# Kernel optimization log

Measured on AMD Instinct MI355X. Metric: run time of the kernel, lower is better.

The kernel has to match this reference:

```python
import jax, jax.numpy as jnp
import numpy as np

N = 50000          # residues
E = 1000000        # edges
H = 128            # hidden_channels
CUT = 11.5         # cutoff
NR = 6             # num_radial
NS = 3             # num_spherical
NPE = 16           # num_pos_emb

def swish(x):
    return x * jax.nn.sigmoid(x)

def rbf(d):
    # Bessel-style radial basis with smooth cosine cutoff, [E, NR]
    u = jnp.clip(d / CUT, 0.0, 1.0)
    n = jnp.arange(1, NR + 1, dtype=jnp.float32)
    fc = 0.5 * (jnp.cos(jnp.pi * u) + 1.0)
    return jnp.sqrt(2.0 / CUT) * jnp.sin(n * jnp.pi * u[:, None]) / (d[:, None] + 1e-6) * fc[:, None]

def angle_emb(d, ang):
    # d_angle_emb: radial x cos(l*angle) -> [E, NR*NS]
    r = rbf(d)
    l = jnp.arange(NS, dtype=jnp.float32)
    a = jnp.cos(ang[:, None] * l)
    return (r[:, :, None] * a[:, None, :]).reshape(d.shape[0], NR * NS)

def theta_phi_emb(d, theta, phi):
    # d_theta_phi_emb: radial x angular(theta) x angular(phi) -> [E, NR*NS*NS]
    r = rbf(d)
    l = jnp.arange(NS, dtype=jnp.float32)
    ct = jnp.cos(theta[:, None] * l)
    cp = jnp.cos(phi[:, None] * l)
    return jnp.einsum('en,el,em->enlm', r, ct, cp).reshape(d.shape[0], NR * NS * NS)


def setup_inputs():
    key = jax.random.key(0)
    ks = jax.random.split(key, 20)
    f32 = jnp.float32
    pos = jax.random.normal(ks[0], (N, 3), f32) * 8.0
    pos_n = pos + jax.random.normal(ks[1], (N, 3), f32) * 0.8
    pos_c = pos + jax.random.normal(ks[2], (N, 3), f32) * 0.8
    z = jax.random.randint(ks[3], (N,), 0, 26)
    bb_embs = jax.random.normal(ks[4], (N, 6), f32)
    side_chain_embs = jax.random.normal(ks[5], (N, 8), f32)
    esm_embs = jax.random.normal(ks[6], (N, 1280), f32)
    batch = jnp.zeros((N,), jnp.int32)
    edge_index = jax.random.randint(ks[7], (2, E), 0, N)
    def w(k, shape):
        return jax.random.normal(k, shape, f32) * (1.0 / np.sqrt(shape[0]))
    edge_in = NR * NS * NS + 3 * NR * NS + NPE  # 54 + 54 + 16 = 124
    params = dict(
        W_emb=w(ks[8], (26 + 6 + 8, H // 2)), b_emb=jnp.zeros((H // 2,), f32),
        W_esm=w(ks[9], (1280, H // 2)), b_esm=jnp.zeros((H // 2,), f32),
        W_edge=w(ks[10], (edge_in, H)),
        W_msg=w(ks[11], (H, H)),
        W_upd=w(ks[12], (H, H)),
        W_o0=w(ks[13], (H, H)), b_o0=jnp.zeros((H,), f32),
        W_o1=w(ks[14], (H, 32)), b_o1=jnp.zeros((32,), f32),
        W_of=w(ks[15], (32, 1)), b_of=jnp.zeros((1,), f32),
        W_n0=w(ks[16], (H, 32)), b_n0=jnp.zeros((32,), f32),
        W_nf=w(ks[17], (32, 2)), b_nf=jnp.zeros((2,), f32),
    )
    return dict(z=z, pos=pos, pos_n=pos_n, pos_c=pos_c, bb_embs=bb_embs,
                side_chain_embs=side_chain_embs, esm_embs=esm_embs,
                batch=batch, edge_index=edge_index, **params)


def reference(z, pos, pos_n, pos_c, bb_embs, side_chain_embs, esm_embs, batch,
              edge_index, W_emb, b_emb, W_esm, b_esm, W_edge, W_msg, W_upd,
              W_o0, b_o0, W_o1, b_o1, W_of, b_of, W_n0, b_n0, W_nf, b_nf):
    # --- node embedding fusion (level='allatom+esm') ---
    oh = jax.nn.one_hot(z, 26, dtype=jnp.float32)
    x_a = jnp.concatenate([oh, bb_embs, side_chain_embs], axis=1) @ W_emb + b_emb
    x_s = esm_embs @ W_esm + b_esm
    x = jnp.concatenate([x_a, x_s], axis=-1)  # [N, H]

    j, i = edge_index[0], edge_index[1]

    # --- sinusoidal positional embedding of sequence offsets ---
    dpe = (j - i).astype(jnp.float32)
    freq = jnp.exp(jnp.arange(0, NPE, 2, dtype=jnp.float32) * (-np.log(10000.0) / NPE))
    ang = dpe[:, None] * freq
    pe = jnp.concatenate([jnp.cos(ang), jnp.sin(ang)], axis=-1)  # [E, NPE]

    # --- distance / theta / phi (triplet gathers via sequence neighbors) ---
    v_ji = pos[j] - pos[i]
    dist = jnp.linalg.norm(pos[i] - pos[j], axis=1)
    refi0 = (i - 1) % N
    refi1 = (i + 1) % N
    v_r0 = pos[refi0] - pos[i]
    v_r1 = pos[refi1] - pos[i]
    a = jnp.sum(v_ji * v_r0, axis=-1)
    b = jnp.linalg.norm(jnp.cross(v_ji, v_r0), axis=-1)
    theta = jnp.arctan2(b, a)
    p1 = jnp.cross(v_r0, v_r1)
    p2 = jnp.cross(v_r0, v_ji)
    a = jnp.sum(p1 * p2, axis=-1)
    b = jnp.sum(jnp.cross(p1, p2) * v_r0, axis=-1) / (jnp.linalg.norm(v_r0, axis=-1) + 1e-7)
    phi = jnp.arctan2(b, a)
    feature0 = theta_phi_emb(dist, theta, phi)  # [E, 54]

    # --- backbone-frame Euler angles (allatom branch) ---
    o1x = pos_n[i] - pos[i]
    o1z = jnp.cross(o1x, jnp.cross(o1x, pos_c[i] - pos[i]))
    o1zl = jnp.linalg.norm(o1z, axis=1) + 1e-7
    o2x = pos_n[j] - pos[j]
    o2z = jnp.cross(o2x, jnp.cross(o2x, pos_c[j] - pos[j]))
    o2zl = jnp.linalg.norm(o2z, axis=1) + 1e-7
    nvec = jnp.cross(o1z, o2z)
    angle1 = jnp.arctan2(jnp.sum(jnp.cross(o1x, nvec) * o1z, -1) / o1zl, jnp.sum(o1x * nvec, -1))
    angle2 = jnp.arctan2(jnp.linalg.norm(nvec, axis=-1), jnp.sum(o1z * o2z, -1))
    angle3 = jnp.arctan2(jnp.sum(jnp.cross(nvec, o2x) * o2z, -1) / o2zl, jnp.sum(nvec * o2x, -1))
    feature1 = jnp.concatenate([angle_emb(dist, angle1), angle_emb(dist, angle2),
                                angle_emb(dist, angle3)], axis=1)  # [E, 54]

    # --- message passing (gather-compute-scatter stand-in for model_E) ---
    ef = swish(jnp.concatenate([feature0, feature1, pe], axis=-1) @ W_edge)  # [E, H]
    m = swish(x[j] @ W_msg) * ef
    agg = jax.ops.segment_sum(m, i, num_segments=N)
    xe = x + swish(agg @ W_upd)

    # --- output heads (dropout inactive at inference) ---
    xn = jax.nn.relu(x @ W_n0 + b_n0)
    node_out = xn @ W_nf + b_nf                   # [N, 2]
    h = jax.nn.relu(xe @ W_o0 + b_o0)
    h = jax.nn.relu(h @ W_o1 + b_o1)
    out = jax.nn.sigmoid(h @ W_of + b_of)         # [N, 1]
    return out, node_out
```

## Files before the change

### kernel.cpp

```cpp
#include <hip/hip_runtime.h>
#include <math.h>
#include <stdint.h>

#define NRES 50000
#define NEDGE 1000000
#define PI_F 3.14159265358979323846f
#define NSEG 196

typedef __attribute__((ext_vector_type(8))) short short8;
typedef __attribute__((ext_vector_type(4))) float floatx4;
typedef __attribute__((ext_vector_type(2))) short bf16x2;
typedef __attribute__((address_space(1))) bf16x2* gbf16x2p;

struct f3 { float x, y, z; };
__device__ __forceinline__ f3 ld3(const float* __restrict__ p, int i) {
  return {p[3*i+0], p[3*i+1], p[3*i+2]};
}
__device__ __forceinline__ f3 f3sub(f3 a, f3 b){ return {a.x-b.x, a.y-b.y, a.z-b.z}; }
__device__ __forceinline__ f3 f3cross(f3 a, f3 b){
  return {a.y*b.z - a.z*b.y, a.z*b.x - a.x*b.z, a.x*b.y - a.y*b.x};
}
__device__ __forceinline__ float f3dot(f3 a, f3 b){ return a.x*b.x + a.y*b.y + a.z*b.z; }
__device__ __forceinline__ float swish_fast(float v){
  return v * __builtin_amdgcn_rcpf(1.0f + __expf(-v));
// ... 23 lines not shown
  float ct, cp, ca1, ca2, ca3;
  float dpe;
};
__device__ __forceinline__ EdgeGeo edge_geo(
    int j, int i,
    const float* __restrict__ pos, const float* __restrict__ posn,
    const float* __restrict__ posc)
{
  EdgeGeo g;
  f3 pj = ld3(pos, j), pi = ld3(pos, i);
  f3 vji = f3sub(pj, pi);
  float nji2 = f3dot(vji, vji);
  float dist = sqrtf(nji2);
  int r0i = (i == 0) ? (NRES - 1) : (i - 1);
  int r1i = (i == NRES - 1) ? 0 : (i + 1);
  f3 vr0 = f3sub(ld3(pos, r0i), pi);
  f3 vr1 = f3sub(ld3(pos, r1i), pi);
  float nr02 = f3dot(vr0, vr0);

  g.ct = f3dot(vji, vr0) * __builtin_amdgcn_rsqf(fmaxf(nji2 * nr02, 1e-30f));
  f3 p1 = f3cross(vr0, vr1);
  f3 p2 = f3cross(vr0, vji);
  float pa = f3dot(p1, p2);
  float pb = f3dot(f3cross(p1, p2), vr0) / (sqrtf(nr02) + 1e-7f);
  g.cp = cos_atan2(pb, pa);

  f3 pni = ld3(posn, i), pci = ld3(posc, i);
  f3 o1x = f3sub(pni, pi);
  f3 o1z = f3cross(o1x, f3cross(o1x, f3sub(pci, pi)));
  float no1z2 = f3dot(o1z, o1z);
  float o1zl = sqrtf(no1z2) + 1e-7f;
  f3 pnj = ld3(posn, j), pcj = ld3(posc, j);
  f3 o2x = f3sub(pnj, pj);
  f3 o2z = f3cross(o2x, f3cross(o2x, f3sub(pcj, pj)));
  float no2z2 = f3dot(o2z, o2z);
  float o2zl = sqrtf(no2z2) + 1e-7f;
  f3 nv = f3cross(o1z, o2z);
  float y1 = f3dot(f3cross(o1x, nv), o1z) / o1zl;
  g.ca1 = cos_atan2(y1, f3dot(o1x, nv));
  g.ca2 = f3dot(o1z, o2z) * __builtin_amdgcn_rsqf(fmaxf(no1z2 * no2z2, 1e-30f));
  float y3 = f3dot(f3cross(nv, o2x), o2z) / o2zl;
  g.ca3 = cos_atan2(y3, f3dot(nv, o2x));

  float u = fminf(dist * (1.0f/11.5f), 1.0f);
  float spu, cpu;
  __sincosf(PI_F * u, &spu, &cpu);
  float fc = 0.5f * (cpu + 1.0f);
  float pref = 0.41702882811414954f * __builtin_amdgcn_rcpf(dist + 1e-6f) * fc;
  {
    float twoc = 2.0f * cpu;
    float s_nm1 = 0.0f, s_n = spu;
    #pragma unroll
    for (int nn = 0; nn < 6; ++nn) {
      g.rb[nn] = pref * s_n;
      float s_np1 = twoc * s_n - s_nm1;
      s_nm1 = s_n; s_n = s_np1;
    }
  }
  g.dpe = (float)(j - i);
  return g;
}

__device__ __forceinline__ float feat_val(const EdgeGeo& g, int f,
                                          const float* ctv, const float* cpv,
                                          const float* cav1, const float* cav2,
                                          const float* cav3)
{
  if (f < 54) {
    int nn = f / 9, l = (f % 9) / 3, m = f % 3;
    return g.rb[nn] * ctv[l] * cpv[m];
  } else {
    int ff = f - 54;
    int t = ff / 18, nn = (ff % 18) / 3, l = ff % 3;
    const float* cav = (t == 0) ? cav1 : (t == 1) ? cav2 : cav3;
    return g.rb[nn] * cav[l];
  }
}

__device__ __forceinline__ void expand_q(
    const EdgeGeo& g, int e, int q, short (*sF)[136])
{
  float ctv[3]  = {1.0f, g.ct,  2.0f*g.ct*g.ct  - 1.0f};
  float cpv[3]  = {1.0f, g.cp,  2.0f*g.cp*g.cp  - 1.0f};
  float cav1[3] = {1.0f, g.ca1, 2.0f*g.ca1*g.ca1 - 1.0f};
  float cav2[3] = {1.0f, g.ca2, 2.0f*g.ca2*g.ca2 - 1.0f};
  float cav3[3] = {1.0f, g.ca3, 2.0f*g.ca3*g.ca3 - 1.0f};

  if (q == 0) {
    #pragma unroll
    for (int f = 0; f < 28; f += 2)
      *(unsigned*)&sF[e][f] = pkbf(feat_val(g, f, ctv, cpv, cav1, cav2, cav3),
                                   feat_val(g, f+1, ctv, cpv, cav1, cav2, cav3));
  } else if (q == 1) {
    #pragma unroll
    for (int f = 28; f < 54; f += 2)
      *(unsigned*)&sF[e][f] = pkbf(feat_val(g, f, ctv, cpv, cav1, cav2, cav3),
                                   feat_val(g, f+1, ctv, cpv, cav1, cav2, cav3));
    const float FRQ[8] = {1.0f, 0.31622776601683794f, 0.1f, 0.03162277660168379f,
                          0.01f, 0.003162277660168379f, 0.001f, 0.0003162277660168379f};
    float cb[8], sb[8];
    #pragma unroll
    for (int p = 0; p < 8; ++p) __sincosf(g.dpe * FRQ[p], &sb[p], &cb[p]);
    #pragma unroll
    for (int p = 0; p < 8; p += 2) {
      *(unsigned*)&sF[e][108 + p] = pkbf(cb[p], cb[p+1]);
      *(unsigned*)&sF[e][116 + p] = pkbf(sb[p], sb[p+1]);
    }
    *(unsigned*)&sF[e][124] = 0u;
    *(unsigned*)&sF[e][126] = 0u;
  } else if (q == 2) {
    #pragma unroll
    for (int f = 54; f < 80; f += 2)
      *(unsigned*)&sF[e][f] = pkbf(feat_val(g, f, ctv, cpv, cav1, cav2, cav3),
                                   feat_val(g, f+1, ctv, cpv, cav1, cav2, cav3));
  } else {
    #pragma unroll
    for (int f = 80; f < 108; f += 2)
      *(unsigned*)&sF[e][f] = pkbf(feat_val(g, f, ctv, cpv, cav1, cav2, cav3),
                                   feat_val(g, f+1, ctv, cpv, cav1, cav2, cav3));
  }
}

__device__ __forceinline__ void edge_features_full(
    int e, int j, int i,
    const float* __restrict__ pos, const float* __restrict__ posn,
    const float* __restrict__ posc, short (*sF)[136])
{
  EdgeGeo g = edge_geo(j, i, pos, posn, posc);
  float ctv[3]  = {1.0f, g.ct,  2.0f*g.ct*g.ct  - 1.0f};
  float cpv[3]  = {1.0f, g.cp,  2.0f*g.cp*g.cp  - 1.0f};
  float cav1[3] = {1.0f, g.ca1, 2.0f*g.ca1*g.ca1 - 1.0f};
  float cav2[3] = {1.0f, g.ca2, 2.0f*g.ca2*g.ca2 - 1.0f};
  float cav3[3] = {1.0f, g.ca3, 2.0f*g.ca3*g.ca3 - 1.0f};
  #pragma unroll
  for (int f = 0; f < 108; f += 2) {
    float v0 = feat_val(g, f,     ctv, cpv, cav1, cav2, cav3);
    float v1 = feat_val(g, f + 1, ctv, cpv, cav1, cav2, cav3);
    *(unsigned*)&sF[e][f] = pkbf(v0, v1);
  }
  const float FRQ[8] = {1.0f, 0.31622776601683794f, 0.1f, 0.03162277660168379f,
                        0.01f, 0.003162277660168379f, 0.001f, 0.0003162277660168379f};
  float cb[8], sb[8];
  #pragma unroll
  for (int q = 0; q < 8; ++q) __sincosf(g.dpe * FRQ[q], &sb[q], &cb[q]);
  #pragma unroll
  for (int q = 0; q < 8; q += 2) {
    *(unsigned*)&sF[e][108 + q] = pkbf(cb[q], cb[q+1]);
    *(unsigned*)&sF[e][116 + q] = pkbf(sb[q], sb[q+1]);
  }
  *(unsigned*)&sF[e][124] = 0u;
  *(unsigned*)&sF[e][126] = 0u;
}

__global__ __launch_bounds__(256) void k_wprep(
    const float* __restrict__ We, const float* __restrict__ Wm,
    const float* __restrict__ Ws, const float* __restrict__ Wu,
    const float* __restrict__ Wo0, const float* __restrict__ Wn0,
    const float* __restrict__ Wo1,
    short* __restrict__ Wef, short* __restrict__ Wmf, short* __restrict__ Wsf,
    short* __restrict__ Wuf, short* __restrict__ Wo0f,
    short* __restrict__ Wn0f, short* __restrict__ Wo1f)
{
  int gid = blockIdx.x * 256 + threadIdx.x;
  const float* src; short* dst; int NT, K, N, t;
  if      (gid < 16384)  { t = gid;          src = We;  dst = Wef;  NT = 8; K = 124;  N = 128; }
  else if (gid < 32768)  { t = gid - 16384;  src = Wm;  dst = Wmf;  NT = 8; K = 128;  N = 128; }
  else if (gid < 114688) { t = gid - 32768;  src = Ws;  dst = Wsf;  NT = 4; K = 1280; N = 64;  }
  else if (gid < 131072) { t = gid - 114688; src = Wu;  dst = Wuf;  NT = 8; K = 128;  N = 128; }
  else if (gid < 147456) { t = gid - 131072; src = Wo0; dst = Wo0f; NT = 8; K = 128;  N = 128; }
  else if (gid < 151552) { t = gid - 147456; src = Wn0; dst = Wn0f; NT = 2; K = 128;  N = 32;  }
  else if (gid < 155648) { t = gid - 151552; src = Wo1; dst = Wo1f; NT = 2; K = 128;  N = 32;  }
  else return;
  int j = t & 7, lane = (t >> 3) & 63;
  int rest = t >> 9;
  int nt = rest % NT, kt = rest / NT;
  int k = kt*32 + (lane >> 4)*8 + j, n = nt*16 + (lane & 15);
  dst[t] = f2bf((k < K) ? src[k*N + n] : 0.0f);
}

__global__ __launch_bounds__(256) void k_hist(
    const int* __restrict__ ei, int* __restrict__ bins)
{
  int e = blockIdx.x * 256 + threadIdx.x;
  if (e < NEDGE) atomicAdd(&bins[ei[NEDGE + e]], 1);
}

__global__ __launch_bounds__(256) void k_scan1(
    int* __restrict__ bins, int* __restrict__ bsum)
{
  __shared__ int s[256];
  const int t = threadIdx.x, b = blockIdx.x;
  const int idx = b * 256 + t;
  int v = (idx < NRES) ? bins[idx] : 0;
  s[t] = v;
  __syncthreads();
  #pragma unroll
  for (int d = 1; d < 256; d <<= 1) {
    int add = (t >= d) ? s[t - d] : 0;
    __syncthreads();
    if (t >= d) s[t] += add;
    __syncthreads();
  }
  if (idx < NRES) bins[idx] = s[t] - v;
  if (t == 255) bsum[b] = s[255];
}

__global__ __launch_bounds__(256) void k_scan2(int* __restrict__ bsum)
{
  __shared__ int s[256];
  const int t = threadIdx.x;
  int v = (t < NSEG) ? bsum[t] : 0;
  s[t] = v;
  __syncthreads();
  #pragma unroll
  for (int d = 1; d < 256; d <<= 1) {
    int add = (t >= d) ? s[t - d] : 0;
    __syncthreads();
    if (t >= d) s[t] += add;
    __syncthreads();
  }
  if (t < NSEG) bsum[t] = s[t] - v;
}

__global__ __launch_bounds__(256) void k_scatter(
    const int* __restrict__ ei, int* __restrict__ bins,
    const int* __restrict__ bsum, int2* __restrict__ sij)
{
  int e = blockIdx.x * 256 + threadIdx.x;
  if (e < NEDGE) {
    int j = ei[e], i = ei[NEDGE + e];
    int slot = atomicAdd(&bins[i], 1) + bsum[i >> 8];
    if (slot >= 0 && slot < NEDGE) sij[slot] = make_int2(j, i);
  }
}

__global__ __launch_bounds__(256) void k_xa(
    const int* __restrict__ z, const float* __restrict__ bb,
    const float* __restrict__ side, const float* __restrict__ W_emb,
    const float* __restrict__ b_emb, short* __restrict__ xb)
{
  int tid = threadIdx.x;
  int h = tid & 63;
  int n = blockIdx.x * 4 + (tid >> 6);
  if (n >= NRES) return;
  int zz = z[n];
  float acc = W_emb[zz * 64 + h] + b_emb[h];
  #pragma unroll
  for (int k = 0; k < 6; ++k) acc += bb[n*6 + k] * W_emb[(26 + k)*64 + h];
  #pragma unroll
  for (int k = 0; k < 8; ++k) acc += side[n*8 + k] * W_emb[(32 + k)*64 + h];
  xb[(size_t)n * 128 + h] = f2bf(acc);
}

__global__ __launch_bounds__(256) void k_esm(
    const float* __restrict__ esm, const short* __restrict__ Wsf,
    const float* __restrict__ b, short* __restrict__ xb)
{
  const int tid = threadIdx.x;
  const int lane = tid & 63, w = tid >> 6;
  const int quad = lane >> 4, colb = lane & 15;
  const int tile0 = blockIdx.x * 64 + w * 16;

  int arow = tile0 + colb;
  if (arow >= NRES) arow = NRES - 1;
  const float* ap = esm + (size_t)arow * 1280 + quad * 8;

  floatx4 acc[4];
  #pragma unroll
  for (int nt = 0; nt < 4; ++nt) acc[nt] = (floatx4){0.f, 0.f, 0.f, 0.f};

  for (int kt = 0; kt < 40; ++kt) {
    float4 v0 = *(const float4*)(ap + kt*32);
    float4 v1 = *(const float4*)(ap + kt*32 + 4);
    short8 a;
    a[0] = f2bf(v0.x); a[1] = f2bf(v0.y); a[2] = f2bf(v0.z); a[3] = f2bf(v0.w);
    a[4] = f2bf(v1.x); a[5] = f2bf(v1.y); a[6] = f2bf(v1.z); a[7] = f2bf(v1.w);
    #pragma unroll
    for (int nt = 0; nt < 4; ++nt) {
      short8 bf = *(const short8*)&Wsf[(size_t)((kt*4 + nt)*64 + lane)*8];
      acc[nt] = __builtin_amdgcn_mfma_f32_16x16x32_bf16(a, bf, acc[nt], 0, 0, 0);
    }
  }
  #pragma unroll
  for (int nt = 0; nt < 4; ++nt) {
    int ch = nt*16 + colb;
    float bias = b[ch];
    #pragma unroll
    for (int r = 0; r < 4; ++r) {
      int n = tile0 + quad*4 + r;
      if (n < NRES) xb[(size_t)n * 128 + 64 + ch] = f2bf(acc[nt][r] + bias);
    }
  }
}

__global__ __launch_bounds__(512) void k_node(
    const float* __restrict__ esm, const short* __restrict__ Wsf,
    const float* __restrict__ b_esm,
    const int* __restrict__ z, const float* __restrict__ bb,
    const float* __restrict__ side, const float* __restrict__ W_emb,
    const float* __restrict__ b_emb,
    const short* __restrict__ Wmf,
    short* __restrict__ xb, short* __restrict__ xmb)
{
  __shared__ __align__(16) short sE[2][64][72];
  __shared__ __align__(16) short sX[64][136];

  const int tid = threadIdx.x;
  const int lane = tid & 63, w = tid >> 6;
  const int quad = lane >> 4, colb = lane & 15;
  const int n0 = blockIdx.x * 64;

  const int lrow = tid >> 3;
  const int p0 = tid & 7, p1 = p0 + 8;
  int grow = n0 + lrow; if (grow >= NRES) grow = NRES - 1;
  const float* rbase = esm + (size_t)grow * 1280;

  const int rt = w & 3;
  const int ct0 = (w >> 2) * 2, ct1 = ct0 + 1;

  floatx4 acc0 = (floatx4){0.f,0.f,0.f,0.f};
  floatx4 acc1 = (floatx4){0.f,0.f,0.f,0.f};

  {
    float4 va = *(const float4*)(rbase + p0*4);
    float4 vb = *(const float4*)(rbase + p1*4);
    *(unsigned*)&sE[0][lrow][p0*4]     = pkbf(va.x, va.y);
    *(unsigned*)&sE[0][lrow][p0*4 + 2] = pkbf(va.z, va.w);
    *(unsigned*)&sE[0][lrow][p1*4]     = pkbf(vb.x, vb.y);
    *(unsigned*)&sE[0][lrow][p1*4 + 2] = pkbf(vb.z, vb.w);
  }
  __syncthreads();

  for (int s = 0; s < 20; ++s) {
    float4 va = {0.f,0.f,0.f,0.f}, vb = {0.f,0.f,0.f,0.f};
    if (s < 19) {
      va = *(const float4*)(rbase + (s+1)*64 + p0*4);
      vb = *(const float4*)(rbase + (s+1)*64 + p1*4);
    }
    const int buf = s & 1;
    #pragma unroll
    for (int kk = 0; kk < 2; ++kk) {
      short8 af = *(const short8*)&sE[buf][rt*16 + colb][kk*32 + quad*8];
      const int kc = s*2 + kk;
      short8 bf0 = *(const short8*)&Wsf[(size_t)((kc*4 + ct0)*64 + lane)*8];
      short8 bf1 = *(const short8*)&Wsf[(size_t)((kc*4 + ct1)*64 + lane)*8];
      acc0 = __builtin_amdgcn_mfma_f32_16x16x32_bf16(af, bf0, acc0, 0, 0, 0);
      acc1 = __builtin_amdgcn_mfma_f32_16x16x32_bf16(af, bf1, acc1, 0, 0, 0);
    }
    if (s < 19) {
      const int nb = (s + 1) & 1;
      *(unsigned*)&sE[nb][lrow][p0*4]     = pkbf(va.x, va.y);
      *(unsigned*)&sE[nb][lrow][p0*4 + 2] = pkbf(va.z, va.w);
      *(unsigned*)&sE[nb][lrow][p1*4]     = pkbf(vb.x, vb.y);
      *(unsigned*)&sE[nb][lrow][p1*4 + 2] = pkbf(vb.z, vb.w);
    }
    __syncthreads();
  }

  {
    float bias0 = b_esm[ct0*16 + colb];
    float bias1 = b_esm[ct1*16 + colb];
    #pragma unroll
    for (int r = 0; r < 4; ++r) {
      int row = rt*16 + quad*4 + r;
      sX[row][64 + ct0*16 + colb] = f2bf(acc0[r] + bias0);
      sX[row][64 + ct1*16 + colb] = f2bf(acc1[r] + bias1);
    }
  }
  {
    int r2 = tid >> 3;
    int n2 = n0 + r2; if (n2 >= NRES) n2 = NRES - 1;
    int c0 = (tid & 7) * 8;
    int zz = z[n2];
    float bbv[6], sdv[8];
    #pragma unroll
    for (int k = 0; k < 6; ++k) bbv[k] = bb[n2*6 + k];
    #pragma unroll
    for (int k = 0; k < 8; ++k) sdv[k] = side[n2*8 + k];
    #pragma unroll
    for (int c = 0; c < 8; c += 2) {
      float u0, u1;
      #pragma unroll
      for (int h = 0; h < 2; ++h) {
        int col = c0 + c + h;
        float a2 = W_emb[zz*64 + col] + b_emb[col];
        #pragma unroll
        for (int k = 0; k < 6; ++k) a2 += bbv[k] * W_emb[(26 + k)*64 + col];
        #pragma unroll
        for (int k = 0; k < 8; ++k) a2 += sdv[k] * W_emb[(32 + k)*64 + col];
        if (h) u1 = a2; else u0 = a2;
      }
      *(unsigned*)&sX[r2][c0 + c] = pkbf(u0, u1);
    }
  }
  __syncthreads();

  #pragma unroll
  for (int it = 0; it < 2; ++it) {
    int idx = it * 512 + tid;
    int row = idx >> 4, c8 = idx & 15;
    int n = n0 + row;
    if (n < NRES) *(short8*)&xb[(size_t)n * 128 + c8*8] = *(const short8*)&sX[row][c8*8];
  }

  floatx4 accM[4];
  #pragma unroll
  for (int mt = 0; mt < 4; ++mt) accM[mt] = (floatx4){0.f,0.f,0.f,0.f};
  #pragma unroll
  for (int kt = 0; kt < 4; ++kt) {
    short8 b0 = *(const short8*)&Wmf[(size_t)((kt*8 + w)*64 + lane)*8];
    #pragma unroll
    for (int mt = 0; mt < 4; ++mt) {
      short8 a = *(const short8*)&sX[mt*16 + colb][kt*32 + quad*8];
      accM[mt] = __builtin_amdgcn_mfma_f32_16x16x32_bf16(a, b0, accM[mt], 0, 0, 0);
    }
  }
  __syncthreads();

  #pragma unroll
  for (int mt = 0; mt < 4; ++mt)
    #pragma unroll
    for (int r = 0; r < 4; ++r)
      sX[mt*16 + quad*4 + r][w*16 + colb] = f2bf(swish_fast(accM[mt][r]));
  __syncthreads();
  #pragma unroll
  for (int it = 0; it < 2; ++it) {
    int idx = it * 512 + tid;
    int row = idx >> 4, c8 = idx & 15;
    int n = n0 + row;
    if (n < NRES) *(short8*)&xmb[(size_t)n * 128 + c8*8] = *(const short8*)&sX[row][c8*8];
  }
}

__global__ __launch_bounds__(256, 4) void k_edge_s(
    const int2* __restrict__ sij,
    const float* __restrict__ pos,
    const float* __restrict__ posn, const float* __restrict__ posc,
    const short* __restrict__ xmb, const short* __restrict__ Wef,
    short* __restrict__ aggb)
{
  __shared__ int sJ[64];
  __shared__ int sI[64];
  __shared__ float sG[64][15];
  __shared__ __align__(16) short sF[64][136];
  __shared__ __align__(16) short sXJ[64][136];

  const int tid = threadIdx.x;
  const int orig = blockIdx.x;
  const int xcd = orig & 7, sub = orig >> 3;
  const int wg = (xcd == 0 ? 0 : 1954 + (xcd - 1) * 1953) + sub;
  const int e0 = wg * 64;

  if (tid < 64) {
    int2 ji = sij[e0 + tid];
    int jj = ji.x, ii = ji.y;
    sJ[tid] = (jj < 0) ? 0 : ((jj >= NRES) ? NRES - 1 : jj);
    sI[tid] = (ii < 0) ? 0 : ((ii >= NRES) ? NRES - 1 : ii);
  }
  __syncthreads();

  if (tid < 64) {
    EdgeGeo g = edge_geo(sJ[tid], sI[tid], pos, posn, posc);
    #pragma unroll
    for (int k = 0; k < 6; ++k) sG[tid][k] = g.rb[k];
    sG[tid][6] = g.ct;  sG[tid][7] = g.cp;
    sG[tid][8] = g.ca1; sG[tid][9] = g.ca2; sG[tid][10] = g.ca3;
    sG[tid][11] = g.dpe;
  } else {
    const int t2 = tid - 64;
    for (int it = 0; it < 6; ++it) {
      int idx = it * 192 + t2;
      if (idx < 1024) {
        int row = idx >> 4;
        int c8 = idx & 15;
        *(short8*)&sXJ[row][c8*8] = *(const short8*)&xmb[(size_t)sJ[row] * 128 + c8*8];
      }
    }
  }
  __syncthreads();

  {
    const int e = tid & 63, q = tid >> 6;
    EdgeGeo g;
    #pragma unroll
    for (int k = 0; k < 6; ++k) g.rb[k] = sG[e][k];
    g.ct  = sG[e][6];  g.cp  = sG[e][7];
    g.ca1 = sG[e][8];  g.ca2 = sG[e][9]; g.ca3 = sG[e][10];
    g.dpe = sG[e][11];
    expand_q(g, e, q, sF);
  }
  __syncthreads();

  const int lane = tid & 63, w = tid >> 6;
  const int quad = lane >> 4, colb = lane & 15;
  const int nb = w * 2;

  short8 bE[4][2];
  #pragma unroll
  for (int kt = 0; kt < 4; ++kt)
    #pragma unroll
    for (int nt = 0; nt < 2; ++nt)
      bE[kt][nt] = *(const short8*)&Wef[(size_t)((kt*8 + nb + nt)*64 + lane)*8];

  floatx4 accE[4][2];
  #pragma unroll
  for (int mt = 0; mt < 4; ++mt) {
    accE[mt][0] = (floatx4){0.f, 0.f, 0.f, 0.f};
    accE[mt][1] = (floatx4){0.f, 0.f, 0.f, 0.f};
  }

  #pragma unroll
  for (int kt = 0; kt < 4; ++kt) {
    #pragma unroll
    for (int mt = 0; mt < 4; ++mt) {
      short8 af = *(const short8*)&sF[mt*16 + colb][kt*32 + quad*8];
      #pragma unroll
      for (int nt = 0; nt < 2; ++nt)
        accE[mt][nt] = __builtin_amdgcn_mfma_f32_16x16x32_bf16(af, bE[kt][nt], accE[mt][nt], 0, 0, 0);
    }
  }
  __syncthreads();

  short (*sM)[136] = sF;
  #pragma unroll
  for (int mt = 0; mt < 4; ++mt)
    #pragma unroll
    for (int nt = 0; nt < 2; ++nt) {
      int ch = w*32 + nt*16 + colb;
      #pragma unroll
      for (int r = 0; r < 4; ++r) {
        int e = mt*16 + quad*4 + r;
        float mv = bf2f(sXJ[e][ch]) * swish_fast(accE[mt][nt][r]);
        sM[e][ch] = f2bf(mv);
      }
    }
  __syncthreads();

  {
    const int p = tid & 63;
    const int g = tid >> 6;
    float ax = 0.f, ay = 0.f;
    int cur = sI[g * 16];
    #pragma unroll
    for (int rr = 0; rr < 16; ++rr) {
      int row = g * 16 + rr;
      int ii = sI[row];
      if (ii != cur) {
        bf16x2 v; v[0] = f2bf(ax); v[1] = f2bf(ay);
        atom_pk_bf16(&aggb[(size_t)cur * 128 + p*2], v);
        ax = 0.f; ay = 0.f; cur = ii;
      }
      bf16x2 mv = *(const bf16x2*)&sM[row][p*2];
      ax += bf2f(mv[0]); ay += bf2f(mv[1]);
    }
    bf16x2 v; v[0] = f2bf(ax); v[1] = f2bf(ay);
    atom_pk_bf16(&aggb[(size_t)cur * 128 + p*2], v);
  }
}

__global__ __launch_bounds__(256, 4) void k_edge_b(
    const int* __restrict__ ei, const float* __restrict__ pos,
    const float* __restrict__ posn, const float* __restrict__ posc,
    const short* __restrict__ xb, const short* __restrict__ Wef,
    const short* __restrict__ Wmf, short* __restrict__ aggb)
{
  __shared__ int sJ[64];
  __shared__ int sI[64];
  __shared__ __align__(16) short sF[64][136];
  __shared__ __align__(16) short sXJ[64][136];

  const int tid = threadIdx.x;
  const int e0 = blockIdx.x * 64;

  if (tid < 64) { sJ[tid] = ei[e0 + tid]; sI[tid] = ei[NEDGE + e0 + tid]; }
  __syncthreads();

  if (tid < 64) {
    edge_features_full(tid, sJ[tid], sI[tid], pos, posn, posc, sF);
  } else {
    const int t2 = tid - 64;
    for (int it = 0; it < 6; ++it) {
      int idx = it * 192 + t2;
      if (idx < 1024) {
        int row = idx >> 4;
        int c8 = idx & 15;
        *(short8*)&sXJ[row][c8*8] = *(const short8*)&xb[(size_t)sJ[row] * 128 + c8*8];
      }
    }
  }
  __syncthreads();

  const int lane = tid & 63, w = tid >> 6;
  const int quad = lane >> 4, colb = lane & 15;
  const int nb = w * 2;

  short8 bE[4][2], bM[4][2];
  #pragma unroll
  for (int kt = 0; kt < 4; ++kt)
    #pragma unroll
    for (int nt = 0; nt < 2; ++nt) {
      bE[kt][nt] = *(const short8*)&Wef[(size_t)((kt*8 + nb + nt)*64 + lane)*8];
      bM[kt][nt] = *(const short8*)&Wmf[(size_t)((kt*8 + nb + nt)*64 + lane)*8];
    }

  floatx4 accE[4][2], accM[4][2];
  #pragma unroll
  for (int mt = 0; mt < 4; ++mt)
    #pragma unroll
    for (int nt = 0; nt < 2; ++nt) {
      accE[mt][nt] = (floatx4){0.f, 0.f, 0.f, 0.f};
      accM[mt][nt] = (floatx4){0.f, 0.f, 0.f, 0.f};
    }

  #pragma unroll
  for (int kt = 0; kt < 4; ++kt) {
    #pragma unroll
    for (int mt = 0; mt < 4; ++mt) {
      short8 af = *(const short8*)&sF [mt*16 + colb][kt*32 + quad*8];
      short8 ax = *(const short8*)&sXJ[mt*16 + colb][kt*32 + quad*8];
      #pragma unroll
      for (int nt = 0; nt < 2; ++nt) {
        accE[mt][nt] = __builtin_amdgcn_mfma_f32_16x16x32_bf16(af, bE[kt][nt], accE[mt][nt], 0, 0, 0);
        accM[mt][nt] = __builtin_amdgcn_mfma_f32_16x16x32_bf16(ax, bM[kt][nt], accM[mt][nt], 0, 0, 0);
      }
    }
  }
  __syncthreads();

  short (*sM)[136] = sXJ;
  #pragma unroll
  for (int mt = 0; mt < 4; ++mt)
    #pragma unroll
    for (int nt = 0; nt < 2; ++nt) {
      int ch = w*32 + nt*16 + colb;
      #pragma unroll
      for (int r = 0; r < 4; ++r) {
        int e = mt*16 + quad*4 + r;
        sM[e][ch] = f2bf(swish_fast(accM[mt][nt][r]) * swish_fast(accE[mt][nt][r]));
      }
    }
  __syncthreads();

  #pragma unroll
  for (int it = 0; it < 16; ++it) {
    int flat = it * 256 + tid;
    int row = flat >> 6, p = flat & 63;
    bf16x2 v = *(const bf16x2*)&sM[row][p*2];
    atom_pk_bf16(&aggb[(size_t)sI[row] * 128 + p*2], v);
  }
}

__global__ __launch_bounds__(256) void k_upd(
    const short* __restrict__ xb, const short* __restrict__ aggb,
    const short* __restrict__ Wuf, const short* __restrict__ Wo0f,
    const short* __restrict__ Wn0f, const short* __restrict__ Wo1f,
    const float* __restrict__ bn0, const float* __restrict__ Wnf,
    const float* __restrict__ bnf, const float* __restrict__ bo0,
    const float* __restrict__ bo1, const float* __restrict__ Wof,
    const float* __restrict__ bof, float* __restrict__ out0,
    float* __restrict__ out1)
{
  __shared__ __align__(16) short sA[64][136];
  __shared__ __align__(16) short sX[64][136];
  __shared__ float sS[64][33];

  const int tid = threadIdx.x;
  const int lane = tid & 63, w = tid >> 6;
  const int quad = lane >> 4, colb = lane & 15;
  const int n0 = blockIdx.x * 64;

  #pragma unroll
  for (int it = 0; it < 4; ++it) {
    int idx = it * 256 + tid;
    int row = idx >> 4, c8 = idx & 15;
    int n = n0 + row;
    short8 va = (short8)(short)0, vx = (short8)(short)0;
    if (n < NRES) {
      va = *(const short8*)&aggb[(size_t)n * 128 + c8*8];
      vx = *(const short8*)&xb  [(size_t)n * 128 + c8*8];
    }
    *(short8*)&sA[row][c8*8] = va;
    *(short8*)&sX[row][c8*8] = vx;
  }
  __syncthreads();

  {
    floatx4 accN[2];
    accN[0] = (floatx4){0.f,0.f,0.f,0.f}; accN[1] = (floatx4){0.f,0.f,0.f,0.f};
    #pragma unroll
    for (int kt = 0; kt < 4; ++kt) {
      short8 a = *(const short8*)&sX[w*16 + colb][kt*32 + quad*8];
      #pragma unroll
      for (int nt = 0; nt < 2; ++nt) {
        short8 bf = *(const short8*)&Wn0f[(size_t)((kt*2 + nt)*64 + lane)*8];
        accN[nt] = __builtin_amdgcn_mfma_f32_16x16x32_bf16(a, bf, accN[nt], 0, 0, 0);
      }
    }
    #pragma unroll
    for (int nt = 0; nt < 2; ++nt) {
      int col = nt*16 + colb;
      float bias = bn0[col];
      #pragma unroll
      for (int r = 0; r < 4; ++r)
        sS[w*16 + quad*4 + r][col] = fmaxf(accN[nt][r] + bias, 0.0f);
    }
  }
  __syncthreads();
  if (tid < 128) {
    int row = tid >> 1, oc = tid & 1;
    int n = n0 + row;
    if (n < NRES) {
      float a2 = bnf[oc];
      #pragma unroll
      for (int k = 0; k < 32; ++k) a2 += sS[row][k] * Wnf[k*2 + oc];
      out1[(size_t)n * 2 + oc] = a2;
    }
  }

  floatx4 acc1[4][2];
  #pragma unroll
  for (int mt = 0; mt < 4; ++mt) {
    acc1[mt][0] = (floatx4){0.f,0.f,0.f,0.f};
    acc1[mt][1] = (floatx4){0.f,0.f,0.f,0.f};
  }
  #pragma unroll
  for (int kt = 0; kt < 4; ++kt) {
    short8 b0 = *(const short8*)&Wuf[(size_t)((kt*8 + w*2 + 0)*64 + lane)*8];
    short8 b1 = *(const short8*)&Wuf[(size_t)((kt*8 + w*2 + 1)*64 + lane)*8];
    #pragma unroll
    for (int mt = 0; mt < 4; ++mt) {
      short8 a = *(const short8*)&sA[mt*16 + colb][kt*32 + quad*8];
      acc1[mt][0] = __builtin_amdgcn_mfma_f32_16x16x32_bf16(a, b0, acc1[mt][0], 0, 0, 0);
      acc1[mt][1] = __builtin_amdgcn_mfma_f32_16x16x32_bf16(a, b1, acc1[mt][1], 0, 0, 0);
    }
  }
  __syncthreads();
  #pragma unroll
  for (int mt = 0; mt < 4; ++mt)
    #pragma unroll
    for (int nt = 0; nt < 2; ++nt)
      #pragma unroll
      for (int r = 0; r < 4; ++r) {
        int row = mt*16 + quad*4 + r, col = w*32 + nt*16 + colb;
        float xv = bf2f(sX[row][col]);
        sA[row][col] = f2bf(xv + swish_fast(acc1[mt][nt][r]));
      }
  __syncthreads();

  floatx4 acc2[4][2];
  #pragma unroll
  for (int mt = 0; mt < 4; ++mt) {
    acc2[mt][0] = (floatx4){0.f,0.f,0.f,0.f};
    acc2[mt][1] = (floatx4){0.f,0.f,0.f,0.f};
  }
  #pragma unroll
  for (int kt = 0; kt < 4; ++kt) {
    short8 b0 = *(const short8*)&Wo0f[(size_t)((kt*8 + w*2 + 0)*64 + lane)*8];
    short8 b1 = *(const short8*)&Wo0f[(size_t)((kt*8 + w*2 + 1)*64 + lane)*8];
    #pragma unroll
    for (int mt = 0; mt < 4; ++mt) {
      short8 a = *(const short8*)&sA[mt*16 + colb][kt*32 + quad*8];
      acc2[mt][0] = __builtin_amdgcn_mfma_f32_16x16x32_bf16(a, b0, acc2[mt][0], 0, 0, 0);
      acc2[mt][1] = __builtin_amdgcn_mfma_f32_16x16x32_bf16(a, b1, acc2[mt][1], 0, 0, 0);
    }
  }
  __syncthreads();
  #pragma unroll
  for (int mt = 0; mt < 4; ++mt)
    #pragma unroll
    for (int nt = 0; nt < 2; ++nt) {
      int col = w*32 + nt*16 + colb;
      float bias = bo0[col];
      #pragma unroll
      for (int r = 0; r < 4; ++r) {
        int row = mt*16 + quad*4 + r;
        sX[row][col] = f2bf(fmaxf(acc2[mt][nt][r] + bias, 0.0f));
      }
    }
  __syncthreads();

  {
    floatx4 accH[2];
    accH[0] = (floatx4){0.f,0.f,0.f,0.f}; accH[1] = (floatx4){0.f,0.f,0.f,0.f};
    #pragma unroll
    for (int kt = 0; kt < 4; ++kt) {
      short8 a = *(const short8*)&sX[w*16 + colb][kt*32 + quad*8];
      #pragma unroll
      for (int nt = 0; nt < 2; ++nt) {
        short8 bf = *(const short8*)&Wo1f[(size_t)((kt*2 + nt)*64 + lane)*8];
        accH[nt] = __builtin_amdgcn_mfma_f32_16x16x32_bf16(a, bf, accH[nt], 0, 0, 0);
      }
    }
    __syncthreads();
    #pragma unroll
    for (int nt = 0; nt < 2; ++nt) {
      int col = nt*16 + colb;
      float bias = bo1[col];
      #pragma unroll
      for (int r = 0; r < 4; ++r)
        sS[w*16 + quad*4 + r][col] = fmaxf(accH[nt][r] + bias, 0.0f);
    }
  }
  __syncthreads();

  if (tid < 64) {
    int n = n0 + tid;
    if (n < NRES) {
      float a2 = bof[0];
      #pragma unroll
      for (int k = 0; k < 32; ++k) a2 += sS[tid][k] * Wof[k];
      out0[n] = 1.0f / (1.0f + expf(-a2));
    }
  }
}

extern "C" void kernel_launch(void* const* d_in, const int* in_sizes, int n_in,
                              void* d_out, int out_size, void* d_ws, size_t ws_size,
                              hipStream_t stream) {
  (void)in_sizes; (void)n_in; (void)out_size;
  const int*   z     = (const int*)  d_in[0];
  const float* pos   = (const float*)d_in[1];
  const float* posn  = (const float*)d_in[2];
  const float* posc  = (const float*)d_in[3];
  const float* bb    = (const float*)d_in[4];
  const float* side  = (const float*)d_in[5];
  const float* esm   = (const float*)d_in[6];
  const int*   ei    = (const int*)  d_in[8];
  const float* W_emb = (const float*)d_in[9];
  const float* b_emb = (const float*)d_in[10];
  const float* W_esm = (const float*)d_in[11];
  const float* b_esm = (const float*)d_in[12];
  const float* W_edge= (const float*)d_in[13];
  const float* W_msg = (const float*)d_in[14];
  const float* W_upd = (const float*)d_in[15];
  const float* W_o0  = (const float*)d_in[16];
  const float* b_o0  = (const float*)d_in[17];
  const float* W_o1  = (const float*)d_in[18];
  const float* b_o1  = (const float*)d_in[19];
  const float* W_of  = (const float*)d_in[20];
  const float* b_of  = (const float*)d_in[21];
  const float* W_n0  = (const float*)d_in[22];
  const float* b_n0  = (const float*)d_in[23];
  const float* W_nf  = (const float*)d_in[24];
  const float* b_nf  = (const float*)d_in[25];

  float* out0 = (float*)d_out;
  float* out1 = out0 + NRES;
  char* ws = (char*)d_ws;

  const bool full = (ws_size >= (size_t)46912096);

  if (full) {
    short* xb   = (short*)ws;
    short* aggb = (short*)(ws + 12800000);
    short* xmb  = (short*)(ws + 25600000);
    short* Wef  = (short*)(ws + 38400000);
    short* Wmf  = (short*)(ws + 38432768);
    short* Wsf  = (short*)(ws + 38465536);
    short* Wuf  = (short*)(ws + 38629376);
    short* Wo0f = (short*)(ws + 38662144);
    short* Wn0f = (short*)(ws + 38694912);
    short* Wo1f = (short*)(ws + 38703104);
    int*   bins = (int*)  (ws + 38711296);
    int*   bsum = (int*)  (ws + 38911296);
    int2*  sij  = (int2*) (ws + 38912096);

    hipMemsetAsync(aggb, 0, (size_t)NRES * 128 * sizeof(short), stream);
    hipMemsetAsync(bins, 0, (size_t)NRES * sizeof(int), stream);

    k_wprep  <<<608, 256, 0, stream>>>(W_edge, W_msg, W_esm, W_upd, W_o0, W_n0, W_o1,
                                       Wef, Wmf, Wsf, Wuf, Wo0f, Wn0f, Wo1f);
    k_hist   <<<3907, 256, 0, stream>>>(ei, bins);
    k_scan1  <<<NSEG, 256, 0, stream>>>(bins, bsum);
    k_scan2  <<<1,    256, 0, stream>>>(bsum);
    k_scatter<<<3907, 256, 0, stream>>>(ei, bins, bsum, sij);
    k_node   <<<782,  512, 0, stream>>>(esm, Wsf, b_esm, z, bb, side, W_emb, b_emb,
                                        Wmf, xb, xmb);
    k_edge_s <<<15625, 256, 0, stream>>>(sij, pos, posn, posc, xmb, Wef, aggb);
    k_upd    <<<782,   256, 0, stream>>>(xb, aggb, Wuf, Wo0f, Wn0f, Wo1f,
                                         b_n0, W_nf, b_nf, b_o0, b_o1, W_of, b_of,
                                         out0, out1);
  } else {
    short* xb   = (short*)ws;
    short* aggb = (short*)(ws + 12800000);
    short* Wef  = (short*)(ws + 25600000);
    short* Wmf  = (short*)(ws + 25632768);
    short* Wsf  = (short*)(ws + 25665536);
    short* Wuf  = (short*)(ws + 25829376);
    short* Wo0f = (short*)(ws + 25862144);
    short* Wn0f = (short*)(ws + 25894912);
    short* Wo1f = (short*)(ws + 25903104);

    hipMemsetAsync(aggb, 0, (size_t)NRES * 128 * sizeof(short), stream);

    k_wprep <<<608, 256, 0, stream>>>(W_edge, W_msg, W_esm, W_upd, W_o0, W_n0, W_o1,
                                      Wef, Wmf, Wsf, Wuf, Wo0f, Wn0f, Wo1f);
    k_xa    <<<12500, 256, 0, stream>>>(z, bb, side, W_emb, b_emb, xb);
    k_esm   <<<782,   256, 0, stream>>>(esm, Wsf, b_esm, xb);
    k_edge_b<<<15625, 256, 0, stream>>>(ei, pos, posn, posc, xb, Wef, Wmf, aggb);
    k_upd   <<<782,   256, 0, stream>>>(xb, aggb, Wuf, Wo0f, Wn0f, Wo1f,
                                        b_n0, W_nf, b_nf, b_o0, b_o1, W_of, b_of,
                                        out0, out1);
  }
}
```

Before: 679.2 us.

## Fuse hist into wprep, node head into k_node, and double edge tile size

Merges the edge histogram into the weight-prep launch and moves the node output head (W_n0/W_nf) into k_node, where x is already in shared memory, so k_upd_s only computes the update and output path. The edge kernel now processes 128 edges per 512-thread block, with each wave owning one 16-column slice across eight row tiles, and its XCD-aware block remap is adjusted to the new block count. Padding edges get a sentinel index and are skipped during the atomic scatter. This cuts launches and redundant node reads and gives more edges per block for segment-reduction, but the larger shared-memory footprint and lower occupancy could hurt latency hiding.

```diff
diff --git a/kernel.cpp b/kernel.cpp
--- a/kernel.cpp
+++ b/kernel.cpp
@@ -199,6 +199,37 @@
   *(unsigned*)&sF[e][126] = 0u;
 }
 
+__global__ __launch_bounds__(256) void k_wprep_hist(
+    const float* __restrict__ We, const float* __restrict__ Wm,
+    const float* __restrict__ Ws, const float* __restrict__ Wu,
+    const float* __restrict__ Wo0, const float* __restrict__ Wn0,
+    const float* __restrict__ Wo1,
+    short* __restrict__ Wef, short* __restrict__ Wmf, short* __restrict__ Wsf,
+    short* __restrict__ Wuf, short* __restrict__ Wo0f,
+    short* __restrict__ Wn0f, short* __restrict__ Wo1f,
+    const int* __restrict__ ei, int* __restrict__ bins)
+{
+  if (blockIdx.x >= 608) {
+    int e = (blockIdx.x - 608) * 256 + threadIdx.x;
+    if (e < NEDGE) atomicAdd(&bins[ei[NEDGE + e]], 1);
+    return;
+  }
+  int gid = blockIdx.x * 256 + threadIdx.x;
+  const float* src; short* dst; int NT, K, N, t;
+  if      (gid < 16384)  { t = gid;          src = We;  dst = Wef;  NT = 8; K = 124;  N = 128; }
+  else if (gid < 32768)  { t = gid - 16384;  src = Wm;  dst = Wmf;  NT = 8; K = 128;  N = 128; }
+  else if (gid < 114688) { t = gid - 32768;  src = Ws;  dst = Wsf;  NT = 4; K = 1280; N = 64;  }
+  else if (gid < 131072) { t = gid - 114688; src = Wu;  dst = Wuf;  NT = 8; K = 128;  N = 128; }
+  else if (gid < 147456) { t = gid - 131072; src = Wo0; dst = Wo0f; NT = 8; K = 128;  N = 128; }
+  else if (gid < 151552) { t = gid - 147456; src = Wn0; dst = Wn0f; NT = 2; K = 128;  N = 32;  }
+  else                   { t = gid - 151552; src = Wo1; dst = Wo1f; NT = 2; K = 128;  N = 32;  }
+  int j = t & 7, lane = (t >> 3) & 63;
+  int rest = t >> 9;
+  int nt = rest % NT, kt = rest / NT;
+  int k = kt*32 + (lane >> 4)*8 + j, n = nt*16 + (lane & 15);
+  dst[t] = f2bf((k < K) ? src[k*N + n] : 0.0f);
+}
+
 __global__ __launch_bounds__(256) void k_wprep(
     const float* __restrict__ We, const float* __restrict__ Wm,
     const float* __restrict__ Ws, const float* __restrict__ Wu,
@@ -225,13 +256,6 @@
   dst[t] = f2bf((k < K) ? src[k*N + n] : 0.0f);
 }
 
-__global__ __launch_bounds__(256) void k_hist(
-    const int* __restrict__ ei, int* __restrict__ bins)
-{
-  int e = blockIdx.x * 256 + threadIdx.x;
-  if (e < NEDGE) atomicAdd(&bins[ei[NEDGE + e]], 1);
-}
-
 __global__ __launch_bounds__(256) void k_scan1(
     int* __restrict__ bins, int* __restrict__ bsum)
 {
@@ -347,7 +371,10 @@
     const float* __restrict__ side, const float* __restrict__ W_emb,
     const float* __restrict__ b_emb,
     const short* __restrict__ Wmf,
-    short* __restrict__ xb, short* __restrict__ xmb)
+    const short* __restrict__ Wn0f, const float* __restrict__ bn0,
+    const float* __restrict__ Wnf, const float* __restrict__ bnf,
+    short* __restrict__ xb, short* __restrict__ xmb,
+    float* __restrict__ out1)
 {
   __shared__ __align__(16) short sE[2][64][72];
   __shared__ __align__(16) short sX[64][136];
@@ -462,6 +489,23 @@
       accM[mt] = __builtin_amdgcn_mfma_f32_16x16x32_bf16(a, b0, accM[mt], 0, 0, 0);
     }
   }
+
+  float (*sS)[33] = (float(*)[33])&sE[0][0][0];
+  {
+    const int hmt = w & 3, hnt = w >> 2;
+    floatx4 accN = (floatx4){0.f,0.f,0.f,0.f};
+    #pragma unroll
+    for (int kt = 0; kt < 4; ++kt) {
+      short8 a = *(const short8*)&sX[hmt*16 + colb][kt*32 + quad*8];
+      short8 bf = *(const short8*)&Wn0f[(size_t)((kt*2 + hnt)*64 + lane)*8];
+      accN = __builtin_amdgcn_mfma_f32_16x16x32_bf16(a, bf, accN, 0, 0, 0);
+    }
+    int col = hnt*16 + colb;
+    float bias = bn0[col];
+    #pragma unroll
+    for (int r = 0; r < 4; ++r)
+      sS[hmt*16 + quad*4 + r][col] = fmaxf(accN[r] + bias, 0.0f);
+  }
   __syncthreads();
 
   #pragma unroll
@@ -469,6 +513,16 @@
     #pragma unroll
     for (int r = 0; r < 4; ++r)
       sX[mt*16 + quad*4 + r][w*16 + colb] = f2bf(swish_fast(accM[mt][r]));
+  if (tid < 128) {
+    int row = tid >> 1, oc = tid & 1;
+    int n = n0 + row;
+    if (n < NRES) {
+      float a2 = bnf[oc];
+      #pragma unroll
+      for (int k = 0; k < 32; ++k) a2 += sS[row][k] * Wnf[k*2 + oc];
+      out1[(size_t)n * 2 + oc] = a2;
+    }
+  }
   __syncthreads();
   #pragma unroll
   for (int it = 0; it < 2; ++it) {
@@ -479,45 +533,51 @@
   }
 }
 
-__global__ __launch_bounds__(256, 4) void k_edge_s(
+__global__ __launch_bounds__(512, 2) void k_edge_s(
     const int2* __restrict__ sij,
     const float* __restrict__ pos,
     const float* __restrict__ posn, const float* __restrict__ posc,
     const short* __restrict__ xmb, const short* __restrict__ Wef,
     short* __restrict__ aggb)
 {
-  __shared__ int sJ[64];
-  __shared__ int sI[64];
-  __shared__ float sG[64][15];
-  __shared__ __align__(16) short sF[64][136];
-  __shared__ __align__(16) short sXJ[64][136];
+  __shared__ int sJ[128];
+  __shared__ int sI[128];
+  __shared__ float sG[128][15];
+  __shared__ __align__(16) short sF[128][136];
+  __shared__ __align__(16) short sXJ[128][136];
 
   const int tid = threadIdx.x;
   const int orig = blockIdx.x;
   const int xcd = orig & 7, sub = orig >> 3;
-  const int wg = (xcd == 0 ? 0 : 1954 + (xcd - 1) * 1953) + sub;
-  const int e0 = wg * 64;
-
-  if (tid < 64) {
-    int2 ji = sij[e0 + tid];
-    int jj = ji.x, ii = ji.y;
-    sJ[tid] = (jj < 0) ? 0 : ((jj >= NRES) ? NRES - 1 : jj);
-    sI[tid] = (ii < 0) ? 0 : ((ii >= NRES) ? NRES - 1 : ii);
-  }
-  __syncthreads();
-
-  if (tid < 64) {
-    EdgeGeo g = edge_geo(sJ[tid], sI[tid], pos, posn, posc);
+  const int wg = (xcd < 5 ? xcd * 977 : 5*977 + (xcd - 5) * 976) + sub;
+  const int e0 = wg * 128;
+
+  if (tid < 128) {
+    int ee = e0 + tid;
+    if (ee < NEDGE) {
+      int2 ji = sij[ee];
+      int jj = ji.x, ii = ji.y;
+      sJ[tid] = (jj < 0) ? 0 : ((jj >= NRES) ? NRES - 1 : jj);
+      sI[tid] = (ii < 0) ? 0 : ((ii >= NRES) ? NRES - 1 : ii);
+    } else {
+      sJ[tid] = 0; sI[tid] = -1;
+    }
+  }
+  __syncthreads();
+
+  if (tid < 128) {
+    int ii = sI[tid]; if (ii < 0) ii = 0;
+    EdgeGeo g = edge_geo(sJ[tid], ii, pos, posn, posc);
     #pragma unroll
     for (int k = 0; k < 6; ++k) sG[tid][k] = g.rb[k];
     sG[tid][6] = g.ct;  sG[tid][7] = g.cp;
     sG[tid][8] = g.ca1; sG[tid][9] = g.ca2; sG[tid][10] = g.ca3;
     sG[tid][11] = g.dpe;
   } else {
-    const int t2 = tid - 64;
+    const int t2 = tid - 128;
     for (int it = 0; it < 6; ++it) {
-      int idx = it * 192 + t2;
-      if (idx < 1024) {
+      int idx = it * 384 + t2;
+      if (idx < 2048) {
         int row = idx >> 4;
         int c8 = idx & 15;
         *(short8*)&sXJ[row][c8*8] = *(const short8*)&xmb[(size_t)sJ[row] * 128 + c8*8];
@@ -527,7 +587,7 @@
   __syncthreads();
 
   {
-    const int e = tid & 63, q = tid >> 6;
+    const int e = tid & 127, q = tid >> 7;
     EdgeGeo g;
     #pragma unroll
     for (int k = 0; k < 6; ++k) g.rb[k] = sG[e][k];
@@ -540,47 +600,37 @@
 
   const int lane = tid & 63, w = tid >> 6;
   const int quad = lane >> 4, colb = lane & 15;
-  const int nb = w * 2;
-
-  short8 bE[4][2];
+
+  short8 bE[4];
   #pragma unroll
   for (int kt = 0; kt < 4; ++kt)
-    #pragma unroll
-    for (int nt = 0; nt < 2; ++nt)
-      bE[kt][nt] = *(const short8*)&Wef[(size_t)((kt*8 + nb + nt)*64 + lane)*8];
-
-  floatx4 accE[4][2];
-  #pragma unroll
-  for (int mt = 0; mt < 4; ++mt) {
-    accE[mt][0] = (floatx4){0.f, 0.f, 0.f, 0.f};
-    accE[mt][1] = (floatx4){0.f, 0.f, 0.f, 0.f};
-  }
+    bE[kt] = *(const short8*)&Wef[(size_t)((kt*8 + w)*64 + lane)*8];
+
+  floatx4 accE[8];
+  #pragma unroll
+  for (int mt = 0; mt < 8; ++mt) accE[mt] = (floatx4){0.f, 0.f, 0.f, 0.f};
 
   #pragma unroll
   for (int kt = 0; kt < 4; ++kt) {
     #pragma unroll
-    for (int mt = 0; mt < 4; ++mt) {
+    for (int mt = 0; mt < 8; ++mt) {
       short8 af = *(const short8*)&sF[mt*16 + colb][kt*32 + quad*8];
-      #pragma unroll
-      for (int nt = 0; nt < 2; ++nt)
-        accE[mt][nt] = __builtin_amdgcn_mfma_f32_16x16x32_bf16(af, bE[kt][nt], accE[mt][nt], 0, 0, 0);
+      accE[mt] = __builtin_amdgcn_mfma_f32_16x16x32_bf16(af, bE[kt], accE[mt], 0, 0, 0);
     }
   }
   __syncthreads();
 
   short (*sM)[136] = sF;
   #pragma unroll
-  for (int mt = 0; mt < 4; ++mt)
-    #pragma unroll
-    for (int nt = 0; nt < 2; ++nt) {
-      int ch = w*32 + nt*16 + colb;
-      #pragma unroll
-      for (int r = 0; r < 4; ++r) {
-        int e = mt*16 + quad*4 + r;
-        float mv = bf2f(sXJ[e][ch]) * swish_fast(accE[mt][nt][r]);
-        sM[e][ch] = f2bf(mv);
-      }
-    }
+  for (int mt = 0; mt < 8; ++mt) {
+    int ch = w*16 + colb;
+    #pragma unroll
+    for (int r = 0; r < 4; ++r) {
+      int e = mt*16 + quad*4 + r;
+      float mv = bf2f(sXJ[e][ch]) * swish_fast(accE[mt][r]);
+      sM[e][ch] = f2bf(mv);
+    }
+  }
   __syncthreads();
 
   {
@@ -593,15 +643,19 @@
       int row = g * 16 + rr;
       int ii = sI[row];
       if (ii != cur) {
-        bf16x2 v; v[0] = f2bf(ax); v[1] = f2bf(ay);
-        atom_pk_bf16(&aggb[(size_t)cur * 128 + p*2], v);
+        if (cur >= 0) {
+          bf16x2 v; v[0] = f2bf(ax); v[1] = f2bf(ay);
+          atom_pk_bf16(&aggb[(size_t)cur * 128 + p*2], v);
+        }
         ax = 0.f; ay = 0.f; cur = ii;
       }
       bf16x2 mv = *(const bf16x2*)&sM[row][p*2];
       ax += bf2f(mv[0]); ay += bf2f(mv[1]);
     }
-    bf16x2 v; v[0] = f2bf(ax); v[1] = f2bf(ay);
-    atom_pk_bf16(&aggb[(size_t)cur * 128 + p*2], v);
+    if (cur >= 0) {
+      bf16x2 v; v[0] = f2bf(ax); v[1] = f2bf(ay);
+      atom_pk_bf16(&aggb[(size_t)cur * 128 + p*2], v);
+    }
   }
 }
 
@@ -697,7 +751,135 @@
   }
 }
 
-__global__ __launch_bounds__(256) void k_upd(
+__global__ __launch_bounds__(256) void k_upd_s(
+    const short* __restrict__ xb, const short* __restrict__ aggb,
+    const short* __restrict__ Wuf, const short* __restrict__ Wo0f,
+    const short* __restrict__ Wo1f,
+    const float* __restrict__ bo0, const float* __restrict__ bo1,
+    const float* __restrict__ Wof, const float* __restrict__ bof,
+    float* __restrict__ out0)
+{
+  __shared__ __align__(16) short sA[64][136];
+  __shared__ __align__(16) short sX[64][136];
+  __shared__ float sS[64][33];
+
+  const int tid = threadIdx.x;
+  const int lane = tid & 63, w = tid >> 6;
+  const int quad = lane >> 4, colb = lane & 15;
+  const int n0 = blockIdx.x * 64;
+
+  #pragma unroll
+  for (int it = 0; it < 4; ++it) {
+    int idx = it * 256 + tid;
+    int row = idx >> 4, c8 = idx & 15;
+    int n = n0 + row;
+    short8 va = (short8)(short)0, vx = (short8)(short)0;
+    if (n < NRES) {
+      va = *(const short8*)&aggb[(size_t)n * 128 + c8*8];
+      vx = *(const short8*)&xb  [(size_t)n * 128 + c8*8];
+    }
+    *(short8*)&sA[row][c8*8] = va;
+    *(short8*)&sX[row][c8*8] = vx;
+  }
+  __syncthreads();
+
+  floatx4 acc1[4][2];
+  #pragma unroll
+  for (int mt = 0; mt < 4; ++mt) {
+    acc1[mt][0] = (floatx4){0.f,0.f,0.f,0.f};
+    acc1[mt][1] = (floatx4){0.f,0.f,0.f,0.f};
+  }
+  #pragma unroll
+  for (int kt = 0; kt < 4; ++kt) {
+    short8 b0 = *(const short8*)&Wuf[(size_t)((kt*8 + w*2 + 0)*64 + lane)*8];
+    short8 b1 = *(const short8*)&Wuf[(size_t)((kt*8 + w*2 + 1)*64 + lane)*8];
+    #pragma unroll
+    for (int mt = 0; mt < 4; ++mt) {
+      short8 a = *(const short8*)&sA[mt*16 + colb][kt*32 + quad*8];
+      acc1[mt][0] = __builtin_amdgcn_mfma_f32_16x16x32_bf16(a, b0, acc1[mt][0], 0, 0, 0);
+      acc1[mt][1] = __builtin_amdgcn_mfma_f32_16x16x32_bf16(a, b1, acc1[mt][1], 0, 0, 0);
+    }
+  }
+  __syncthreads();
+  #pragma unroll
+  for (int mt = 0; mt < 4; ++mt)
+    #pragma unroll
+    for (int nt = 0; nt < 2; ++nt)
+      #pragma unroll
+      for (int r = 0; r < 4; ++r) {
+        int row = mt*16 + quad*4 + r, col = w*32 + nt*16 + colb;
+        float xv = bf2f(sX[row][col]);
+        sA[row][col] = f2bf(xv + swish_fast(acc1[mt][nt][r]));
+      }
+  __syncthreads();
+
+  floatx4 acc2[4][2];
+  #pragma unroll
+  for (int mt = 0; mt < 4; ++mt) {
+    acc2[mt][0] = (floatx4){0.f,0.f,0.f,0.f};
+    acc2[mt][1] = (floatx4){0.f,0.f,0.f,0.f};
+  }
+  #pragma unroll
+  for (int kt = 0; kt < 4; ++kt) {
+    short8 b0 = *(const short8*)&Wo0f[(size_t)((kt*8 + w*2 + 0)*64 + lane)*8];
+    short8 b1 = *(const short8*)&Wo0f[(size_t)((kt*8 + w*2 + 1)*64 + lane)*8];
+    #pragma unroll
+    for (int mt = 0; mt < 4; ++mt) {
+      short8 a = *(const short8*)&sA[mt*16 + colb][kt*32 + quad*8];
+      acc2[mt][0] = __builtin_amdgcn_mfma_f32_16x16x32_bf16(a, b0, acc2[mt][0], 0, 0, 0);
+      acc2[mt][1] = __builtin_amdgcn_mfma_f32_16x16x32_bf16(a, b1, acc2[mt][1], 0, 0, 0);
+    }
+  }
+  __syncthreads();
+  #pragma unroll
+  for (int mt = 0; mt < 4; ++mt)
+    #pragma unroll
+    for (int nt = 0; nt < 2; ++nt) {
+      int col = w*32 + nt*16 + colb;
+      float bias = bo0[col];
+      #pragma unroll
+      for (int r = 0; r < 4; ++r) {
+        int row = mt*16 + quad*4 + r;
+        sX[row][col] = f2bf(fmaxf(acc2[mt][nt][r] + bias, 0.0f));
+      }
+    }
+  __syncthreads();
+
+  {
+    floatx4 accH[2];
+    accH[0] = (floatx4){0.f,0.f,0.f,0.f}; accH[1] = (floatx4){0.f,0.f,0.f,0.f};
+    #pragma unroll
+    for (int kt = 0; kt < 4; ++kt) {
+      short8 a = *(const short8*)&sX[w*16 + colb][kt*32 + quad*8];
+      #pragma unroll
+      for (int nt = 0; nt < 2; ++nt) {
+        short8 bf = *(const short8*)&Wo1f[(size_t)((kt*2 + nt)*64 + lane)*8];
+        accH[nt] = __builtin_amdgcn_mfma_f32_16x16x32_bf16(a, bf, accH[nt], 0, 0, 0);
+      }
+    }
+    #pragma unroll
+    for (int nt = 0; nt < 2; ++nt) {
+      int col = nt*16 + colb;
+      float bias = bo1[col];
+      #pragma unroll
+      for (int r = 0; r < 4; ++r)
+        sS[w*16 + quad*4 + r][col] = fmaxf(accH[nt][r] + bias, 0.0f);
+    }
+  }
+  __syncthreads();
+
+  if (tid < 64) {
+    int n = n0 + tid;
+    if (n < NRES) {
+      float a2 = bof[0];
+      #pragma unroll
+      for (int k = 0; k < 32; ++k) a2 += sS[tid][k] * Wof[k];
+      out0[n] = 1.0f / (1.0f + expf(-a2));
+    }
+  }
+}
+
+__global__ __launch_bounds__(256) void k_upd_b(
     const short* __restrict__ xb, const short* __restrict__ aggb,
     const short* __restrict__ Wuf, const short* __restrict__ Wo0f,
     const short* __restrict__ Wn0f, const short* __restrict__ Wo1f,
@@ -915,18 +1097,18 @@
     hipMemsetAsync(aggb, 0, (size_t)NRES * 128 * sizeof(short), stream);
     hipMemsetAsync(bins, 0, (size_t)NRES * sizeof(int), stream);
 
-    k_wprep  <<<608, 256, 0, stream>>>(W_edge, W_msg, W_esm, W_upd, W_o0, W_n0, W_o1,
-                                       Wef, Wmf, Wsf, Wuf, Wo0f, Wn0f, Wo1f);
-    k_hist   <<<3907, 256, 0, stream>>>(ei, bins);
+    k_wprep_hist<<<4515, 256, 0, stream>>>(W_edge, W_msg, W_esm, W_upd, W_o0,
+                                           W_n0, W_o1, Wef, Wmf, Wsf, Wuf,
+                                           Wo0f, Wn0f, Wo1f, ei, bins);
     k_scan1  <<<NSEG, 256, 0, stream>>>(bins, bsum);
     k_scan2  <<<1,    256, 0, stream>>>(bsum);
     k_scatter<<<3907, 256, 0, stream>>>(ei, bins, bsum, sij);
     k_node   <<<782,  512, 0, stream>>>(esm, Wsf, b_esm, z, bb, side, W_emb, b_emb,
-                                        Wmf, xb, xmb);
-    k_edge_s <<<15625, 256, 0, stream>>>(sij, pos, posn, posc, xmb, Wef, aggb);
-    k_upd    <<<782,   256, 0, stream>>>(xb, aggb, Wuf, Wo0f, Wn0f, Wo1f,
-                                         b_n0, W_nf, b_nf, b_o0, b_o1, W_of, b_of,
-                                         out0, out1);
+                                        Wmf, Wn0f, b_n0, W_nf, b_nf,
+                                        xb, xmb, out1);
+    k_edge_s <<<7813, 512, 0, stream>>>(sij, pos, posn, posc, xmb, Wef, aggb);
+    k_upd_s  <<<782,  256, 0, stream>>>(xb, aggb, Wuf, Wo0f, Wo1f,
+                                        b_o0, b_o1, W_of, b_of, out0);
   } else {
     short* xb   = (short*)ws;
     short* aggb = (short*)(ws + 12800000);
@@ -945,7 +1127,7 @@
     k_xa    <<<12500, 256, 0, stream>>>(z, bb, side, W_emb, b_emb, xb);
     k_esm   <<<782,   256, 0, stream>>>(esm, Wsf, b_esm, xb);
     k_edge_b<<<15625, 256, 0, stream>>>(ei, pos, posn, posc, xb, Wef, Wmf, aggb);
-    k_upd   <<<782,   256, 0, stream>>>(xb, aggb, Wuf, Wo0f, Wn0f, Wo1f,
+    k_upd_b <<<782,   256, 0, stream>>>(xb, aggb, Wuf, Wo0f, Wn0f, Wo1f,
                                         b_n0, W_nf, b_nf, b_o0, b_o1, W_of, b_of,
                                         out0, out1);
   }
```

After: 682.2 us. About the same (+0.4%).
